# Performance work log

Measured on AMD Instinct MI355X. Metric: run time of the kernel, lower is better.

The kernel has to match this reference:

```python
import jax, jax.numpy as jnp
import numpy as np

N_FACTORS = 4
N_ITERATIONS = 2
N_LAYERS = 1
DEG_EPS = 1e-8
L2_EPS = 1e-12


def _l2norm(x):
    # torch F.normalize(p=2, dim=1): x / max(||x||, eps)
    n = jnp.sqrt(jnp.sum(x * x, axis=-1, keepdims=True))
    return x / jnp.maximum(n, L2_EPS)


def setup_inputs() -> dict:
    key = jax.random.key(0)
    k1, k2, k3, k4, k5, k6, k7 = jax.random.split(key, 7)
    n_users, n_items, D, M, B = 40000, 20000, 128, 600000, 4096
    return {
        "user_emb": jax.random.normal(k1, (n_users, D), dtype=jnp.float32) * 0.02,
        "item_emb": jax.random.normal(k2, (n_items, D), dtype=jnp.float32) * 0.02,
        "row": jax.random.randint(k3, (M,), 0, n_users, dtype=jnp.int32),
        "col": jax.random.randint(k4, (M,), 0, n_items, dtype=jnp.int32),
        "users": jax.random.randint(k5, (B,), 0, n_users, dtype=jnp.int32),
        "pos": jax.random.randint(k6, (B,), 0, n_items, dtype=jnp.int32),
        "neg": jax.random.randint(k7, (B,), 0, n_items, dtype=jnp.int32),
    }


def reference(user_emb, item_emb, row, col, users, pos, neg):
    n_users = user_emb.shape[0]
    n_nodes = n_users + item_emb.shape[0]
    D = user_emb.shape[1]
    d = D // N_FACTORS

    # symmetric edge list: (u -> i+offset) and (i+offset -> u)
    h = jnp.concatenate([row, col + n_users])  # [E]
    t = jnp.concatenate([col + n_users, row])  # [E]
    E = h.shape[0]

    ego = jnp.concatenate([user_emb, item_emb], axis=0)  # [N, D]
    A = jnp.ones((E, N_FACTORS), dtype=ego.dtype)
    all_emb = [ego]

    for _layer in range(N_LAYERS):
        ego_f = ego.reshape(n_nodes, N_FACTORS, d)  # factor chunks
        factor_emb = None
        for it in range(N_ITERATIONS):
            # build_matrix: per-factor edge softmax + D^-0.5 A D^-0.5
            norm_A = jax.nn.softmax(A, axis=1)                         # [E, F]
            deg = jax.ops.segment_sum(norm_A, h, num_segments=n_nodes)  # [N, F]
            deg = 1.0 / jnp.sqrt(jnp.maximum(deg, DEG_EPS))
            edge_w = norm_A * deg[h] * deg[t]                          # [E, F]
            # per-factor sparse spmm: gather tail, weight, scatter to head
            edge_val = ego_f[t] * edge_w[:, :, None]                   # [E, F, d]
            factor_emb = jax.ops.segment_sum(edge_val, h, num_segments=n_nodes)  # [N, F, d]
            if it < N_ITERATIONS - 1:
                # routing score update (final update is unused by forward)
                hn = _l2norm(factor_emb[h])   # [E, F, d]
                tn = _l2norm(ego_f[t])        # [E, F, d]
                A = A + jnp.sum(hn * jnp.tanh(tn), axis=-1)
        ego = factor_emb.reshape(n_nodes, D)
        all_emb.append(ego)

    out = jnp.mean(jnp.stack(all_emb, axis=1), axis=1)  # [N, D]
    u_g = out[:n_users]
    i_g = out[n_users:]
    return u_g[users], i_g[pos], i_g[neg]
```

## Files before the change

### kernel.cpp

```cpp
#include <hip/hip_runtime.h>
#include <hip/hip_fp16.h>
#include <math.h>

#define NU 40000
#define NI 20000
#define NN 60000
#define DD 128
#define NF 4
#define ME 600000
#define NE 1200000
#define NB 4096
#define NBLK 235
#define CPAD 16


__device__ __forceinline__ const float* node_row(const float* ue, const float* ie, int n) {
    return (n < NU) ? (ue + (size_t)n * DD) : (ie + (size_t)(n - NU) * DD);
}


__global__ void k_zero(int* counts) {
    int i = blockIdx.x * blockDim.x + threadIdx.x;
    if (i < NN * CPAD) counts[i] = 0;
}

__global__ void k_count(const int* __restrict__ row, const int* __restrict__ col,
                        int* __restrict__ counts, int* __restrict__ rank) {
    int base = (blockIdx.x * blockDim.x + threadIdx.x) * 4;
    if (base >= NE) return;
    int4 h4;
    if (base < ME) {
        h4 = *(const int4*)(row + base);
    } else {
        int4 c4 = *(const int4*)(col + (base - ME));
        h4 = make_int4(NU + c4.x, NU + c4.y, NU + c4.z, NU + c4.w);
    }
    int4 r;
    r.x = atomicAdd(&counts[h4.x * CPAD], 1);
    r.y = atomicAdd(&counts[h4.y * CPAD], 1);
    r.z = atomicAdd(&counts[h4.z * CPAD], 1);
    r.w = atomicAdd(&counts[h4.w * CPAD], 1);
    *(int4*)(rank + base) = r;
}


__global__ void k_scanA(const int* __restrict__ counts, int* __restrict__ pre,
                        int* __restrict__ bsum) {
    int tid = threadIdx.x;
    int i = blockIdx.x * 256 + tid;
    int v = (i < NN) ? counts[i * CPAD] : 0;
    int lane = tid & 63, w = tid >> 6;
    int s = v;
    #pragma unroll
    for (int off = 1; off < 64; off <<= 1) {
        int o = __shfl_up(s, off);
        if (lane >= off) s += o;
    }
    __shared__ int wsum[4];
    if (lane == 63) wsum[w] = s;
    __syncthreads();
    int add = 0;
    #pragma unroll
    for (int k = 0; k < 4; ++k) add += (k < w) ? wsum[k] : 0;
    if (i < NN) pre[i] = s - v + add;
    if (tid == 255) bsum[blockIdx.x] = add + s;
}

__global__ void k_scanB(const int* __restrict__ bsum, int* __restrict__ boff) {
    int tid = threadIdx.x;
    int v = (tid < NBLK) ? bsum[tid] : 0;
    int lane = tid & 63, w = tid >> 6;
    int s = v;
    #pragma unroll
    for (int off = 1; off < 64; off <<= 1) {
        int o = __shfl_up(s, off);
        if (lane >= off) s += o;
    }
    __shared__ int wsum[4];
    if (lane == 63) wsum[w] = s;
    __syncthreads();
    int add = 0;
    #pragma unroll
    for (int k = 0; k < 4; ++k) add += (k < w) ? wsum[k] : 0;
    if (tid < NBLK) boff[tid] = s - v + add;
}

__global__ void k_scanC(const int* __restrict__ pre, const int* __restrict__ boff,
                        const int* __restrict__ counts,
                        int* __restrict__ row_ptr, float* __restrict__ dinv0) {
    int i = blockIdx.x * 256 + threadIdx.x;
    if (i < NN) {
        row_ptr[i] = pre[i] + boff[blockIdx.x];
        dinv0[i]   = 1.0f / sqrtf(fmaxf(0.25f * (float)counts[i * CPAD], 1e-8f));
    }
    if (i == 0) row_ptr[NN] = NE;
}

__global__ void k_fill(const int* __restrict__ row, const int* __restrict__ col,
                       const int* __restrict__ row_ptr, const int* __restrict__ rank,
                       unsigned short* __restrict__ t_sorted) {
    int base = (blockIdx.x * blockDim.x + threadIdx.x) * 4;
    if (base >= NE) return;
    int4 h4, t4;
    if (base < ME) {
        h4 = *(const int4*)(row + base);
        int4 c4 = *(const int4*)(col + base);
        t4 = make_int4(NU + c4.x, NU + c4.y, NU + c4.z, NU + c4.w);
    } else {
        int4 c4 = *(const int4*)(col + (base - ME));
        h4 = make_int4(NU + c4.x, NU + c4.y, NU + c4.z, NU + c4.w);
        t4 = *(const int4*)(row + (base - ME));
    }
    int4 r = *(const int4*)(rank + base);
    t_sorted[row_ptr[h4.x] + r.x] = (unsigned short)t4.x;
    t_sorted[row_ptr[h4.y] + r.y] = (unsigned short)t4.y;
    t_sorted[row_ptr[h4.z] + r.z] = (unsigned short)t4.z;
    t_sorted[row_ptr[h4.w] + r.w] = (unsigned short)t4.w;
}

__global__ void k_tohalf(const float* __restrict__ src, __half* __restrict__ dst, int n8) {
    int i = blockIdx.x * blockDim.x + threadIdx.x;
    if (i < n8) {
        float4 a = ((const float4*)src)[2 * i];
        float4 b = ((const float4*)src)[2 * i + 1];
        __half2 h[4] = { __floats2half2_rn(a.x, a.y), __floats2half2_rn(a.z, a.w),
                         __floats2half2_rn(b.x, b.y), __floats2half2_rn(b.z, b.w) };
        ((float4*)dst)[i] = *(float4*)h;
    }
}

__global__ void k_prop0_norm(const float* __restrict__ ue, const float* __restrict__ ie,
                             const __half* __restrict__ ego16,
                             const int* __restrict__ row_ptr,
                             const unsigned short* __restrict__ t_sorted,
                             const float* __restrict__ dinv0,
                             __half* __restrict__ fnorm, __half* __restrict__ ttan) {
    int n = blockIdx.x * 8 + (threadIdx.x >> 5);
    if (n >= NN) return;
    int j = threadIdx.x & 31;
    int p0 = row_ptr[n], p1 = row_ptr[n + 1];
    float4 acc = make_float4(0.f, 0.f, 0.f, 0.f);
    #pragma unroll 4
    for (int p = p0; p < p1; ++p) {
        int t = t_sorted[p];
        float w = dinv0[t];
        float2 raw = ((const float2*)(ego16 + (size_t)t * DD))[j];
        float2 v01 = __half22float2(*(const __half2*)&raw.x);
        float2 v23 = __half22float2(*(const __half2*)&raw.y);
        acc.x += w * v01.x; acc.y += w * v01.y;
        acc.z += w * v23.x; acc.w += w * v23.y;
    }
    float ss = acc.x * acc.x + acc.y * acc.y + acc.z * acc.z + acc.w * acc.w;
    ss += __shfl_xor(ss, 1); ss += __shfl_xor(ss, 2); ss += __shfl_xor(ss, 4);
    float inv = 1.0f / fmaxf(sqrtf(ss), 1e-12f);
    __half2 f01 = __floats2half2_rn(acc.x * inv, acc.y * inv);
    __half2 f23 = __floats2half2_rn(acc.z * inv, acc.w * inv);
    __half2 fpair[2] = { f01, f23 };
    ((float2*)(fnorm + (size_t)n * DD))[j] = *(float2*)fpair;

    float4 u = ((const float4*)node_row(ue, ie, n))[j];
    float s2 = u.x * u.x + u.y * u.y + u.z * u.z + u.w * u.w;
    s2 += __shfl_xor(s2, 1); s2 += __shfl_xor(s2, 2); s2 += __shfl_xor(s2, 4);
    float inv2 = 1.0f / fmaxf(sqrtf(s2), 1e-12f);
    __half2 t01 = __floats2half2_rn(tanhf(u.x * inv2), tanhf(u.y * inv2));
    __half2 t23 = __floats2half2_rn(tanhf(u.z * inv2), tanhf(u.w * inv2));
    __half2 tpair[2] = { t01, t23 };
    ((float2*)(ttan + (size_t)n * DD))[j] = *(float2*)tpair;
}

__global__ void k_attn_deg(const int* __restrict__ row_ptr,
                           const unsigned short* __restrict__ t_sorted,
                           const __half* __restrict__ fnorm, const __half* __restrict__ ttan,
                           float* __restrict__ normA, float* __restrict__ dinv1) {
    int n = blockIdx.x * 4 + (threadIdx.x >> 6);
    if (n >= NN) return;
    int lane = threadIdx.x & 63;
    int g  = lane >> 4;
    int il = lane & 15;
    int f  = il >> 2;
    int p0 = row_ptr[n], p1 = row_ptr[n + 1];
    float4 rawa = ((const float4*)(fnorm + (size_t)n * DD))[il];
    float2 a0 = __half22float2(*(const __half2*)&rawa.x);
    float2 a1 = __half22float2(*(const __half2*)&rawa.y);
    float2 a2 = __half22float2(*(const __half2*)&rawa.z);
    float2 a3 = __half22float2(*(const __half2*)&rawa.w);
    float dacc = 0.0f;
    #pragma unroll 2
    for (int pb = p0; pb < p1; pb += 4) {
        int p = pb + g;
        bool valid = p < p1;
        int pc = valid ? p : (p1 - 1);
        int t = t_sorted[pc];
        float4 raw = ((const float4*)(ttan + (size_t)t * DD))[il];
        float2 b0 = __half22float2(*(const __half2*)&raw.x);
        float2 b1 = __half22float2(*(const __half2*)&raw.y);
        float2 b2 = __half22float2(*(const __half2*)&raw.z);
        float2 b3 = __half22float2(*(const __half2*)&raw.w);
        float s = a0.x * b0.x + a0.y * b0.y + a1.x * b1.x + a1.y * b1.y
                + a2.x * b2.x + a2.y * b2.y + a3.x * b3.x + a3.y * b3.y;
        s += __shfl_xor(s, 1);
        s += __shfl_xor(s, 2);
        float m1 = fmaxf(s, __shfl_xor(s, 4));
        float mx = fmaxf(m1, __shfl_xor(m1, 8));
        float e = __expf(s - mx);
        float sum = e;
        sum += __shfl_xor(sum, 4);
        sum += __shfl_xor(sum, 8);
        float v = e * __builtin_amdgcn_rcpf(sum);
        if (valid) {
            if ((il & 3) == 0) normA[(size_t)pc * 4 + f] = v;
            dacc += v;
        }
    }
    dacc += __shfl_xor(dacc, 16);
    dacc += __shfl_xor(dacc, 32);
    if (g == 0 && (il & 3) == 0)
        dinv1[(size_t)n * 4 + f] = 1.0f / sqrtf(fmaxf(dacc, 1e-8f));
}

__global__ void k_prop1_out(const float* __restrict__ ue, const float* __restrict__ ie,
                            const int* __restrict__ row_ptr,
                            const unsigned short* __restrict__ t_sorted,
                            const float* __restrict__ normA, const float* __restrict__ dinv1,
                            const int* __restrict__ users, const int* __restrict__ pos,
                            const int* __restrict__ neg, float* __restrict__ out) {
    int r = blockIdx.x * 8 + (threadIdx.x >> 5);
    if (r >= 3 * NB) return;
    int j = threadIdx.x & 31;
    int f = j >> 3;
    int which = r >> 12;
    int i = r & 4095;
    int n;
    if (which == 0)      n = users[i];
    else if (which == 1) n = NU + pos[i];
    else                 n = NU + neg[i];
    int p0 = row_ptr[n], p1 = row_ptr[n + 1];
    float4 acc = make_float4(0.f, 0.f, 0.f, 0.f);
    #pragma unroll 4
    for (int p = p0; p < p1; ++p) {
        int t = t_sorted[p];
        float w = normA[(size_t)p * 4 + f] * dinv1[(size_t)t * 4 + f];
        float4 v = ((const float4*)node_row(ue, ie, t))[j];
        acc.x += w * v.x; acc.y += w * v.y;
        acc.z += w * v.z; acc.w += w * v.w;
    }
    float dn = dinv1[(size_t)n * 4 + f];
    float4 e0 = ((const float4*)node_row(ue, ie, n))[j];
    ((float4*)(out + (size_t)r * DD))[j] =
        make_float4(0.5f * (e0.x + dn * acc.x), 0.5f * (e0.y + dn * acc.y),
                    0.5f * (e0.z + dn * acc.z), 0.5f * (e0.w + dn * acc.w));
}


extern "C" void kernel_launch(void* const* d_in, const int* in_sizes, int n_in,
                              void* d_out, int out_size, void* d_ws, size_t ws_size,
                              hipStream_t stream) {
    const float* ue   = (const float*)d_in[0];
    const float* ie   = (const float*)d_in[1];
    const int* row    = (const int*)d_in[2];
    const int* col    = (const int*)d_in[3];
    const int* users  = (const int*)d_in[4];
    const int* pos    = (const int*)d_in[5];
    const int* neg    = (const int*)d_in[6];
    float* out        = (float*)d_out;

    char* ws = (char*)d_ws;
    size_t off = 0;
    auto take = [&](size_t bytes) { void* p = ws + off; off += (bytes + 255) & ~(size_t)255; return p; };
    __half* fnorm    = (__half*)take((size_t)NN * DD * 2);
    __half* ttan     = (__half*)take((size_t)NN * DD * 2);
    __half* ego16    = (__half*)take((size_t)NN * DD * 2);
    float*  normA    = (float*)take((size_t)NE * 4 * 4);
    float*  dinv1    = (float*)take((size_t)NN * 4 * 4);
    float*  dinv0    = (float*)take((size_t)NN * 4);
    int*    row_ptr  = (int*)take((size_t)(NN + 1) * 4);
    int*    counts   = (int*)take((size_t)NN * CPAD * 4);
    int*    pre      = (int*)take((size_t)NN * 4);
    int*    bsum     = (int*)take((size_t)NBLK * 4);
    int*    boff     = (int*)take((size_t)NBLK * 4);
    int*    rank     = (int*)take((size_t)NE * 4);
    unsigned short* t_sorted = (unsigned short*)take((size_t)NE * 2);
    if (off > ws_size) return;

    k_zero <<<(NN * CPAD + 255) / 256, 256, 0, stream>>>(counts);
    k_count<<<(NE / 4 + 255) / 256, 256, 0, stream>>>(row, col, counts, rank);
    k_tohalf<<<((NU * DD / 8) + 255) / 256, 256, 0, stream>>>(ue, ego16, NU * DD / 8);
    k_tohalf<<<((NI * DD / 8) + 255) / 256, 256, 0, stream>>>(ie, ego16 + (size_t)NU * DD, NI * DD / 8);
    k_scanA<<<NBLK, 256, 0, stream>>>(counts, pre, bsum);
    k_scanB<<<1, 256, 0, stream>>>(bsum, boff);
    k_scanC<<<NBLK, 256, 0, stream>>>(pre, boff, counts, row_ptr, dinv0);
    k_fill <<<(NE / 4 + 255) / 256, 256, 0, stream>>>(row, col, row_ptr, rank, t_sorted);
    k_prop0_norm<<<(NN + 7) / 8, 256, 0, stream>>>(ue, ie, ego16, row_ptr, t_sorted,
                                                   dinv0, fnorm, ttan);
    k_attn_deg<<<(NN + 3) / 4, 256, 0, stream>>>(row_ptr, t_sorted, fnorm, ttan,
                                                 normA, (float*)dinv1);
    k_prop1_out<<<(3 * NB) / 8, 256, 0, stream>>>(ue, ie, row_ptr, t_sorted,
                                                  normA, (const float*)dinv1,
                                                  users, pos, neg, out);
}
```

Before: 289.8 us.

## Prescale fp16 embeddings by degree, skip unused normA writes, use fdot2

Folds the per-source inverse-sqrt degree into the fp16 embedding copy, computed after the scan. This drops a dependent dinv0 gather from the first propagation loop. It adds a flag array marking the nodes that are actually queried (users, pos, neg) and writes normA only for those head nodes, which cuts scattered stores. The attention dot product now uses packed fp16 fdot2, and unroll factors are raised. The cost is an extra flag kernel, the conversion now waits on the scan instead of overlapping with it, and fp16 rounding of the scaled values.

```diff
diff --git a/kernel.cpp b/kernel.cpp
--- a/kernel.cpp
+++ b/kernel.cpp
@@ -18,10 +18,32 @@
     return (n < NU) ? (ue + (size_t)n * DD) : (ie + (size_t)(n - NU) * DD);
 }
 
-
-__global__ void k_zero(int* counts) {
+typedef _Float16 hf2_t __attribute__((ext_vector_type(2)));
+__device__ __forceinline__ float fdot2f(unsigned int a, unsigned int b, float c) {
+#if __has_builtin(__builtin_amdgcn_fdot2)
+    return __builtin_amdgcn_fdot2(__builtin_bit_cast(hf2_t, a),
+                                  __builtin_bit_cast(hf2_t, b), c, false);
+#else
+    float2 fa = __half22float2(__builtin_bit_cast(__half2, a));
+    float2 fb = __half22float2(__builtin_bit_cast(__half2, b));
+    return c + fa.x * fb.x + fa.y * fb.y;
+#endif
+}
+
+
+__global__ void k_zero(int* counts, unsigned char* flags) {
     int i = blockIdx.x * blockDim.x + threadIdx.x;
     if (i < NN * CPAD) counts[i] = 0;
+    if (i < NN) flags[i] = 0;
+}
+
+__global__ void k_flag(const int* __restrict__ users, const int* __restrict__ pos,
+                       const int* __restrict__ neg, unsigned char* __restrict__ flags) {
+    int i = blockIdx.x * blockDim.x + threadIdx.x;
+    if (i >= 3 * NB) return;
+    int which = i >> 12, k = i & 4095;
+    int n = (which == 0) ? users[k] : ((which == 1) ? NU + pos[k] : NU + neg[k]);
+    flags[n] = 1;
 }
 
 __global__ void k_count(const int* __restrict__ row, const int* __restrict__ col,
@@ -118,37 +140,39 @@
     t_sorted[row_ptr[h4.w] + r.w] = (unsigned short)t4.w;
 }
 
-__global__ void k_tohalf(const float* __restrict__ src, __half* __restrict__ dst, int n8) {
+__global__ void k_prep(const float* __restrict__ ue, const float* __restrict__ ie,
+                       const float* __restrict__ dinv0, __half* __restrict__ dst) {
     int i = blockIdx.x * blockDim.x + threadIdx.x;
-    if (i < n8) {
-        float4 a = ((const float4*)src)[2 * i];
-        float4 b = ((const float4*)src)[2 * i + 1];
-        __half2 h[4] = { __floats2half2_rn(a.x, a.y), __floats2half2_rn(a.z, a.w),
-                         __floats2half2_rn(b.x, b.y), __floats2half2_rn(b.z, b.w) };
-        ((float4*)dst)[i] = *(float4*)h;
-    }
+    if (i >= NN * DD / 8) return;
+    int n = i >> 4;
+    int off = (i & 15) * 8;
+    const float* src = node_row(ue, ie, n) + off;
+    float w = dinv0[n];
+    float4 a = *(const float4*)src;
+    float4 b = *(const float4*)(src + 4);
+    __half2 h[4] = { __floats2half2_rn(w * a.x, w * a.y), __floats2half2_rn(w * a.z, w * a.w),
+                     __floats2half2_rn(w * b.x, w * b.y), __floats2half2_rn(w * b.z, w * b.w) };
+    ((float4*)dst)[i] = *(float4*)h;
 }
 
 __global__ void k_prop0_norm(const float* __restrict__ ue, const float* __restrict__ ie,
-                             const __half* __restrict__ ego16,
+                             const __half* __restrict__ ego16s,
                              const int* __restrict__ row_ptr,
                              const unsigned short* __restrict__ t_sorted,
-                             const float* __restrict__ dinv0,
                              __half* __restrict__ fnorm, __half* __restrict__ ttan) {
     int n = blockIdx.x * 8 + (threadIdx.x >> 5);
     if (n >= NN) return;
     int j = threadIdx.x & 31;
     int p0 = row_ptr[n], p1 = row_ptr[n + 1];
     float4 acc = make_float4(0.f, 0.f, 0.f, 0.f);
-    #pragma unroll 4
+    #pragma unroll 8
     for (int p = p0; p < p1; ++p) {
         int t = t_sorted[p];
-        float w = dinv0[t];
-        float2 raw = ((const float2*)(ego16 + (size_t)t * DD))[j];
+        float2 raw = ((const float2*)(ego16s + (size_t)t * DD))[j];
         float2 v01 = __half22float2(*(const __half2*)&raw.x);
         float2 v23 = __half22float2(*(const __half2*)&raw.y);
-        acc.x += w * v01.x; acc.y += w * v01.y;
-        acc.z += w * v23.x; acc.w += w * v23.y;
+        acc.x += v01.x; acc.y += v01.y;
+        acc.z += v23.x; acc.w += v23.y;
     }
     float ss = acc.x * acc.x + acc.y * acc.y + acc.z * acc.z + acc.w * acc.w;
     ss += __shfl_xor(ss, 1); ss += __shfl_xor(ss, 2); ss += __shfl_xor(ss, 4);
@@ -171,6 +195,7 @@
 __global__ void k_attn_deg(const int* __restrict__ row_ptr,
                            const unsigned short* __restrict__ t_sorted,
                            const __half* __restrict__ fnorm, const __half* __restrict__ ttan,
+                           const unsigned char* __restrict__ flags,
                            float* __restrict__ normA, float* __restrict__ dinv1) {
     int n = blockIdx.x * 4 + (threadIdx.x >> 6);
     if (n >= NN) return;
@@ -179,25 +204,21 @@
     int il = lane & 15;
     int f  = il >> 2;
     int p0 = row_ptr[n], p1 = row_ptr[n + 1];
-    float4 rawa = ((const float4*)(fnorm + (size_t)n * DD))[il];
-    float2 a0 = __half22float2(*(const __half2*)&rawa.x);
-    float2 a1 = __half22float2(*(const __half2*)&rawa.y);
-    float2 a2 = __half22float2(*(const __half2*)&rawa.z);
-    float2 a3 = __half22float2(*(const __half2*)&rawa.w);
+    bool writeA = flags[n] != 0;
+    uint4 au = ((const uint4*)(fnorm + (size_t)n * DD))[il];
     float dacc = 0.0f;
-    #pragma unroll 2
+    #pragma unroll 4
     for (int pb = p0; pb < p1; pb += 4) {
         int p = pb + g;
         bool valid = p < p1;
         int pc = valid ? p : (p1 - 1);
         int t = t_sorted[pc];
-        float4 raw = ((const float4*)(ttan + (size_t)t * DD))[il];
-        float2 b0 = __half22float2(*(const __half2*)&raw.x);
-        float2 b1 = __half22float2(*(const __half2*)&raw.y);
-        float2 b2 = __half22float2(*(const __half2*)&raw.z);
-        float2 b3 = __half22float2(*(const __half2*)&raw.w);
-        float s = a0.x * b0.x + a0.y * b0.y + a1.x * b1.x + a1.y * b1.y
-                + a2.x * b2.x + a2.y * b2.y + a3.x * b3.x + a3.y * b3.y;
+        uint4 bu = ((const uint4*)(ttan + (size_t)t * DD))[il];
+        float s = 0.0f;
+        s = fdot2f(au.x, bu.x, s);
+        s = fdot2f(au.y, bu.y, s);
+        s = fdot2f(au.z, bu.z, s);
+        s = fdot2f(au.w, bu.w, s);
         s += __shfl_xor(s, 1);
         s += __shfl_xor(s, 2);
         float m1 = fmaxf(s, __shfl_xor(s, 4));
@@ -208,7 +229,7 @@
         sum += __shfl_xor(sum, 8);
         float v = e * __builtin_amdgcn_rcpf(sum);
         if (valid) {
-            if ((il & 3) == 0) normA[(size_t)pc * 4 + f] = v;
+            if (writeA && (il & 3) == 0) normA[(size_t)pc * 4 + f] = v;
             dacc += v;
         }
     }
@@ -269,7 +290,7 @@
     auto take = [&](size_t bytes) { void* p = ws + off; off += (bytes + 255) & ~(size_t)255; return p; };
     __half* fnorm    = (__half*)take((size_t)NN * DD * 2);
     __half* ttan     = (__half*)take((size_t)NN * DD * 2);
-    __half* ego16    = (__half*)take((size_t)NN * DD * 2);
+    __half* ego16s   = (__half*)take((size_t)NN * DD * 2);
     float*  normA    = (float*)take((size_t)NE * 4 * 4);
     float*  dinv1    = (float*)take((size_t)NN * 4 * 4);
     float*  dinv0    = (float*)take((size_t)NN * 4);
@@ -280,20 +301,21 @@
     int*    boff     = (int*)take((size_t)NBLK * 4);
     int*    rank     = (int*)take((size_t)NE * 4);
     unsigned short* t_sorted = (unsigned short*)take((size_t)NE * 2);
+    unsigned char*  flags    = (unsigned char*)take((size_t)NN);
     if (off > ws_size) return;
 
-    k_zero <<<(NN * CPAD + 255) / 256, 256, 0, stream>>>(counts);
+    k_zero <<<(NN * CPAD + 255) / 256, 256, 0, stream>>>(counts, flags);
+    k_flag <<<(3 * NB + 255) / 256, 256, 0, stream>>>(users, pos, neg, flags);
     k_count<<<(NE / 4 + 255) / 256, 256, 0, stream>>>(row, col, counts, rank);
-    k_tohalf<<<((NU * DD / 8) + 255) / 256, 256, 0, stream>>>(ue, ego16, NU * DD / 8);
-    k_tohalf<<<((NI * DD / 8) + 255) / 256, 256, 0, stream>>>(ie, ego16 + (size_t)NU * DD, NI * DD / 8);
     k_scanA<<<NBLK, 256, 0, stream>>>(counts, pre, bsum);
     k_scanB<<<1, 256, 0, stream>>>(bsum, boff);
     k_scanC<<<NBLK, 256, 0, stream>>>(pre, boff, counts, row_ptr, dinv0);
+    k_prep <<<(NN * DD / 8 + 255) / 256, 256, 0, stream>>>(ue, ie, dinv0, ego16s);
     k_fill <<<(NE / 4 + 255) / 256, 256, 0, stream>>>(row, col, row_ptr, rank, t_sorted);
-    k_prop0_norm<<<(NN + 7) / 8, 256, 0, stream>>>(ue, ie, ego16, row_ptr, t_sorted,
-                                                   dinv0, fnorm, ttan);
+    k_prop0_norm<<<(NN + 7) / 8, 256, 0, stream>>>(ue, ie, ego16s, row_ptr, t_sorted,
+                                                   fnorm, ttan);
     k_attn_deg<<<(NN + 3) / 4, 256, 0, stream>>>(row_ptr, t_sorted, fnorm, ttan,
-                                                 normA, (float*)dinv1);
+                                                 flags, normA, (float*)dinv1);
     k_prop1_out<<<(3 * NB) / 8, 256, 0, stream>>>(ue, ie, row_ptr, t_sorted,
                                                   normA, (const float*)dinv1,
                                                   users, pos, neg, out);
```

Result: no change. 286.0 us (-1.3%).
